# Performance work log

Hardware: AMD Instinct MI355X
Metric: run time of the kernel (lower is better)

The kernel has to match this reference:

```python
import jax, jax.numpy as jnp
import numpy as np

N_NODES = 100000
N_EDGES = 1600000
IN_FEATS = 128
HEADS = 4
OUT_FEATS = 32
NEG_SLOPE = 0.2


def setup_inputs() -> dict:
    key = jax.random.key(0)
    ks = jax.random.split(key, 7)
    x = jax.random.normal(ks[0], (N_NODES, IN_FEATS), dtype=jnp.float32)
    fc_w = jax.random.normal(ks[1], (HEADS * OUT_FEATS, IN_FEATS), dtype=jnp.float32) * (1.0 / np.sqrt(IN_FEATS))
    attn_l = jax.random.normal(ks[2], (HEADS, OUT_FEATS), dtype=jnp.float32) * (1.0 / np.sqrt(OUT_FEATS))
    attn_r = jax.random.normal(ks[3], (HEADS, OUT_FEATS), dtype=jnp.float32) * (1.0 / np.sqrt(OUT_FEATS))
    bias = jnp.zeros((HEADS * OUT_FEATS,), dtype=jnp.float32)
    src = jax.random.randint(ks[4], (N_EDGES,), 0, N_NODES, dtype=jnp.int64 if jax.config.jax_enable_x64 else jnp.int32)
    dst = jax.random.randint(ks[5], (N_EDGES,), 0, N_NODES, dtype=jnp.int64 if jax.config.jax_enable_x64 else jnp.int32)
    return {"x": x, "fc_w": fc_w, "attn_l": attn_l, "attn_r": attn_r, "bias": bias, "src": src, "dst": dst}


def reference(x, fc_w, attn_l, attn_r, bias, src, dst):
    """DGL GATConv (feat_drop=attn_drop=0, residual identity since in==H*D,
    allow_zero_in_degree=True, activation=None), then concat heads."""
    N = x.shape[0]
    H, D = attn_l.shape
    # linear projection: [N, H, D]
    feat = (x @ fc_w.T).reshape(N, H, D)
    # per-node attention halves: [N, H]
    el = jnp.einsum('nhd,hd->nh', feat, attn_l)
    er = jnp.einsum('nhd,hd->nh', feat, attn_r)
    # per-edge score with leaky relu: [E, H]
    e = el[src] + er[dst]
    e = jnp.where(e > 0, e, NEG_SLOPE * e)
    # edge softmax grouped by destination node
    emax = jax.ops.segment_max(e, dst, num_segments=N)          # [N, H]
    ee = jnp.exp(e - emax[dst])                                  # [E, H]
    denom = jax.ops.segment_sum(ee, dst, num_segments=N)        # [N, H]
    a = ee / jnp.maximum(denom[dst], jnp.float32(1e-38))         # [E, H]
    # weighted message + scatter aggregate: [N, H, D]
    msg = feat[src] * a[:, :, None]
    rst = jax.ops.segment_sum(msg, dst, num_segments=N)
    # residual (identity since in_feats == H*D) + bias
    rst = rst + x.reshape(N, H, D) + bias.reshape(1, H, D)
    # concat heads
    return rst.reshape(N, H * D)
```

## Files before the change

kernel.cpp:

```cpp
#include <hip/hip_runtime.h>
#include <math.h>

#define NEG_SLOPE 0.2f
#define PB 256
#define BKT_SHIFT 8

typedef __attribute__((ext_vector_type(8))) short bf16x8;
typedef __attribute__((ext_vector_type(4))) float f32x4;

__device__ __forceinline__ unsigned bf16_rne(float f) {
  unsigned u = __float_as_uint(f);
  return (u + 0x7fff + ((u >> 16) & 1)) >> 16;
}

__device__ __forceinline__ float lrelu_exp(float v) {
  v = v > 0.f ? v : NEG_SLOPE * v;
  return __expf(v);
}

__device__ __forceinline__ void local_blk_scan(const int* __restrict__ blk_sums,
                                               int* s_blk_off, int nb, int t) {
  if (t < 64) {
    const int v = (t < nb) ? blk_sums[t] : 0;
    int incl = v;
#pragma unroll
    for (int d = 1; d < 64; d <<= 1) {
      const int o = __shfl_up(incl, d);
      if (t >= d) incl += o;
    }
    s_blk_off[t] = incl - v;
  }
}

__global__ __launch_bounds__(256) void gemm_feat_attn(
    const float* __restrict__ x, const unsigned* __restrict__ fc_wb,
    const float* __restrict__ attn_l, const float* __restrict__ attn_r,
    unsigned* __restrict__ featb, float* __restrict__ el,
    float* __restrict__ er, int N)
{
  __shared__ __align__(16) unsigned w_lds[128 * 68];
  const int t = threadIdx.x;
  const int row_base = blockIdx.x * 64;

  {
    const uint4* fb4 = reinterpret_cast<const uint4*>(fc_wb);
#pragma unroll
    for (int k = 0; k < 8; ++k) {
      const int i4 = t + k * 256;
      const uint4 v = fb4[i4];
      const int row = i4 >> 4;
      unsigned* d = &w_lds[row * 68 + (i4 & 15) * 4];
      d[0] = v.x; d[1] = v.y; d[2] = v.z; d[3] = v.w;
    }
  }

  const int w = t >> 6;
  const int l = t & 63;
  const int cl = l & 15;
  const int g = l >> 4;

  const int arow = min(row_base + w * 16 + cl, N - 1);
  const float* __restrict__ xp = x + (size_t)arow * 128;
  bf16x8 a_frag[4];
#pragma unroll
  for (int ks = 0; ks < 4; ++ks) {
    const float4 v0 = *reinterpret_cast<const float4*>(xp + ks * 32 + g * 8);
    const float4 v1 =
        *reinterpret_cast<const float4*>(xp + ks * 32 + g * 8 + 4);
    uint4 uu;
    uu.x = bf16_rne(v0.x) | (bf16_rne(v0.y) << 16);
    uu.y = bf16_rne(v0.z) | (bf16_rne(v0.w) << 16);
    uu.z = bf16_rne(v1.x) | (bf16_rne(v1.y) << 16);
    uu.w = bf16_rne(v1.z) | (bf16_rne(v1.w) << 16);
    a_frag[ks] = *reinterpret_cast<bf16x8*>(&uu);
  }
  __syncthreads();

  f32x4 acc[8];
#pragma unroll
  for (int ct = 0; ct < 8; ++ct) acc[ct] = (f32x4){0.f, 0.f, 0.f, 0.f};

#pragma unroll
  for (int ct = 0; ct < 8; ++ct) {
#pragma unroll
    for (int ks = 0; ks < 4; ++ks) {
      const bf16x8 b_frag = *reinterpret_cast<const bf16x8*>(
          &w_lds[(ct * 16 + cl) * 68 + ks * 16 + g * 4]);
      acc[ct] = __builtin_amdgcn_mfma_f32_16x16x32_bf16(a_frag[ks], b_frag,
                                                        acc[ct], 0, 0, 0);
    }
  }

#pragma unroll
  for (int ct = 0; ct < 8; ++ct) {
#pragma unroll
    for (int r = 0; r < 4; ++r) {
      const float v = acc[ct][r];
      const float vn = __shfl_xor(v, 1);
      const int node = row_base + w * 16 + g * 4 + r;
      if ((cl & 1) == 0 && node < N) {
        featb[(size_t)node * 64 + ct * 8 + (cl >> 1)] =
            bf16_rne(v) | (bf16_rne(vn) << 16);
      }
    }
  }

  float al_lo[4], al_hi[4], ar_lo[4], ar_hi[4];
#pragma unroll
  for (int h = 0; h < 4; ++h) {
    al_lo[h] = attn_l[h * 32 + cl];
    al_hi[h] = attn_l[h * 32 + 16 + cl];
    ar_lo[h] = attn_r[h * 32 + cl];
    ar_hi[h] = attn_r[h * 32 + 16 + cl];
  }
#pragma unroll
  for (int r = 0; r < 4; ++r) {
    const int node = row_base + w * 16 + g * 4 + r;
#pragma unroll
    for (int h = 0; h < 4; ++h) {
      float pl = acc[2 * h][r] * al_lo[h] + acc[2 * h + 1][r] * al_hi[h];
      float pr = acc[2 * h][r] * ar_lo[h] + acc[2 * h + 1][r] * ar_hi[h];
#pragma unroll
      for (int d = 1; d < 16; d <<= 1) {
        pl += __shfl_xor(pl, d);
        pr += __shfl_xor(pr, d);
      }
      if (cl == 0 && node < N) {
        el[(size_t)node * 4 + h] = pl;
        er[(size_t)node * 4 + h] = pr;
      }
    }
  }
}

__global__ __launch_bounds__(256) void hist_bucket(const int* __restrict__ dst,
                                                   int* __restrict__ hist,
                                                   const float* __restrict__ fc_w,
                                                   unsigned* __restrict__ fc_wb,
                                                   int E, int NB, int chunk) {
  __shared__ int h[512];
  const int k = blockIdx.x, t = threadIdx.x;
  if (k < 32) {
    const int i = k * 256 + t;
    const float2 v = reinterpret_cast<const float2*>(fc_w)[i];
    fc_wb[i] = bf16_rne(v.x) | (bf16_rne(v.y) << 16);
  }
  for (int i = t; i < NB; i += 256) h[i] = 0;
  __syncthreads();
  const int beg = k * chunk, end = min(E, beg + chunk);
  for (int e = beg + t; e < end; e += 256)
    atomicAdd(&h[dst[e] >> BKT_SHIFT], 1);
  __syncthreads();
  for (int i = t; i < NB; i += 256) hist[i * PB + k] = h[i];
}

__global__ __launch_bounds__(256) void scan_a(const int* __restrict__ deg,
                                              int* __restrict__ offs,
                                              int* __restrict__ blk_sums,
                                              int n) {
  __shared__ int wsum[4];
  const int b = blockIdx.x, t = threadIdx.x;
  const int base = b * 2048 + t * 8;
  int v[8];
  int s = 0;
#pragma unroll
  for (int j = 0; j < 8; ++j) {
    v[j] = s;
    const int d = (base + j < n) ? deg[base + j] : 0;
    s += d;
  }
  const int lane = t & 63;
  int incl = s;
#pragma unroll
  for (int d = 1; d < 64; d <<= 1) {
    const int o = __shfl_up(incl, d);
    if (lane >= d) incl += o;
  }
  const int w = t >> 6;
  if (lane == 63) wsum[w] = incl;
  __syncthreads();
  int woff = 0;
  for (int ww = 0; ww < w; ++ww) woff += wsum[ww];
  const int thr_excl = woff + incl - s;
#pragma unroll
  for (int j = 0; j < 8; ++j)
    if (base + j < n) offs[base + j] = thr_excl + v[j];
  if (t == 255) blk_sums[b] = woff + incl;
}

__global__ __launch_bounds__(256) void part_scatter(
    const int* __restrict__ src, const int* __restrict__ dst,
    const int* __restrict__ hscan, const int* __restrict__ blk_sums,
    unsigned* __restrict__ part, int E, int NB, int chunk, int nb) {
  __shared__ int cur[512];
  __shared__ int s_blk_off[64];
  const int k = blockIdx.x, t = threadIdx.x;
  local_blk_scan(blk_sums, s_blk_off, nb, t);
  __syncthreads();
  for (int i = t; i < NB; i += 256) {
    const int m = i * PB + k;
    cur[i] = hscan[m] + s_blk_off[m >> 11];
  }
  __syncthreads();
  const int beg = k * chunk, end = min(E, beg + chunk);
  for (int e = beg + t; e < end; e += 256) {
    const int d = dst[e];
    const int b = d >> BKT_SHIFT;
    const int pos = atomicAdd(&cur[b], 1);
    part[pos] = (unsigned)src[e] |
                ((unsigned)(d & ((1 << BKT_SHIFT) - 1)) << 20);
  }
}

__global__ __launch_bounds__(512) void build_csr(
    const unsigned* __restrict__ part, const int* __restrict__ hscan,
    const int* __restrict__ blk_sums, const float* __restrict__ el,
    const float* __restrict__ er, int* __restrict__ node_offs,
    unsigned* __restrict__ csr, uint2* __restrict__ wsb,
    int N, int E, int NB, int nb) {
  __shared__ int cnt[256];
  __shared__ int wtot[4];
  __shared__ int s_blk_off[64];
  const int b = blockIdx.x, t = threadIdx.x;
  local_blk_scan(blk_sums, s_blk_off, nb, t);
  if (t < 256) cnt[t] = 0;
  __syncthreads();
  const int m0 = b * PB;
  const int bbase = hscan[m0] + s_blk_off[m0 >> 11];
  int bend = E;
  if (b + 1 < NB) {
    const int m1 = (b + 1) * PB;
    bend = hscan[m1] + s_blk_off[m1 >> 11];
  }
  const int node0 = b << BKT_SHIFT;
  for (int p = bbase + t; p < bend; p += 512)
    atomicAdd(&cnt[part[p] >> 20], 1);
  __syncthreads();
  int a0 = 0, incl = 0;
  if (t < 256) {
    a0 = cnt[t];
    incl = a0;
#pragma unroll
    for (int d1 = 1; d1 < 64; d1 <<= 1) {
      const int o = __shfl_up(incl, d1);
      if ((t & 63) >= d1) incl += o;
    }
    if ((t & 63) == 63) wtot[t >> 6] = incl;
  }
  __syncthreads();
  if (t < 256) {
    const int w = t >> 6;
    int woff = 0;
    for (int ww = 0; ww < w; ++ww) woff += wtot[ww];
    const int e0 = woff + incl - a0;
    cnt[t] = e0;
    if (node0 + t < N) node_offs[node0 + t] = bbase + e0;
    if (b == NB - 1 && t == 0) node_offs[N] = E;
  }
  __syncthreads();
  for (int p = bbase + t; p < bend; p += 512) {
    const unsigned v = part[p];
    const int lpos = atomicAdd(&cnt[v >> 20], 1);
    csr[bbase + lpos] = v;
  }
  __syncthreads();
  for (int p = bbase + t; p < bend; p += 512) {
    const unsigned v = csr[p];
    const unsigned s = v & 0xFFFFFu;
    const unsigned ld = v >> 20;
    const float4 l4 = *reinterpret_cast<const float4*>(el + s * 4);
    const float4 r4 =
        *reinterpret_cast<const float4*>(er + (unsigned)(node0 + ld) * 4);
    uint2 u;
    u.x = bf16_rne(lrelu_exp(l4.x + r4.x)) |
          (bf16_rne(lrelu_exp(l4.y + r4.y)) << 16);
    u.y = bf16_rne(lrelu_exp(l4.z + r4.z)) |
          (bf16_rne(lrelu_exp(l4.w + r4.w)) << 16);
    wsb[p] = u;
  }
}

__global__ __launch_bounds__(256) void agg_kernel(
    const uint4* __restrict__ featb4, const unsigned* __restrict__ csr,
    const unsigned short* __restrict__ wsb_us, const float* __restrict__ x,
    const float* __restrict__ bias, const int* __restrict__ node_offs,
    float* __restrict__ out, int N, int E)
{
  const int n = (int)((blockIdx.x * (size_t)blockDim.x + threadIdx.x) >> 6);
  if (n >= N) return;
  const unsigned lane = threadIdx.x & 63;
  const unsigned q = lane >> 4;
  const unsigned li = lane & 15;
  const unsigned hh = li >> 2;
  const unsigned short* __restrict__ wp = wsb_us + hh;
  const int beg = node_offs[n];
  const int end = node_offs[n + 1];
  const int nfull = (end - beg) >> 4;

  float a0 = 0.f, a1 = 0.f, a2 = 0.f, a3 = 0.f;
  float a4 = 0.f, a5 = 0.f, a6 = 0.f, a7 = 0.f, ds = 0.f;
  int p = beg;
  for (int gi = 0; gi < nfull; ++gi, p += 16) {
    unsigned pk[4]; unsigned wu[4]; uint4 fv[4];
#pragma unroll
    for (int i = 0; i < 4; ++i) pk[i] = csr[(unsigned)p + 4 * i + q];
#pragma unroll
    for (int i = 0; i < 4; ++i)
      wu[i] = wp[((unsigned)p + 4 * i + q) * 4];
#pragma unroll
    for (int i = 0; i < 4; ++i)
      fv[i] = featb4[(pk[i] & 0xFFFFFu) * 16 + li];
#pragma unroll
    for (int i = 0; i < 4; ++i) {
      const float w = __uint_as_float(wu[i] << 16);
      a0 = fmaf(w, __uint_as_float(fv[i].x << 16), a0);
      a1 = fmaf(w, __uint_as_float(fv[i].x & 0xffff0000u), a1);
      a2 = fmaf(w, __uint_as_float(fv[i].y << 16), a2);
      a3 = fmaf(w, __uint_as_float(fv[i].y & 0xffff0000u), a3);
      a4 = fmaf(w, __uint_as_float(fv[i].z << 16), a4);
      a5 = fmaf(w, __uint_as_float(fv[i].z & 0xffff0000u), a5);
      a6 = fmaf(w, __uint_as_float(fv[i].w << 16), a6);
      a7 = fmaf(w, __uint_as_float(fv[i].w & 0xffff0000u), a7);
      ds += w;
    }
  }
  if (p < end) {
    const int last = end - 1;
    unsigned pk[4]; unsigned wu[4]; uint4 fv[4]; int ee[4];
#pragma unroll
    for (int i = 0; i < 4; ++i) ee[i] = p + 4 * i + (int)q;
#pragma unroll
    for (int i = 0; i < 4; ++i) pk[i] = csr[(unsigned)min(ee[i], last)];
#pragma unroll
    for (int i = 0; i < 4; ++i)
      wu[i] = wp[(unsigned)min(ee[i], last) * 4];
#pragma unroll
    for (int i = 0; i < 4; ++i)
      fv[i] = featb4[(pk[i] & 0xFFFFFu) * 16 + li];
#pragma unroll
    for (int i = 0; i < 4; ++i) {
      float w = __uint_as_float(wu[i] << 16);
      if (ee[i] > last) w = 0.f;
      a0 = fmaf(w, __uint_as_float(fv[i].x << 16), a0);
      a1 = fmaf(w, __uint_as_float(fv[i].x & 0xffff0000u), a1);
      a2 = fmaf(w, __uint_as_float(fv[i].y << 16), a2);
      a3 = fmaf(w, __uint_as_float(fv[i].y & 0xffff0000u), a3);
      a4 = fmaf(w, __uint_as_float(fv[i].z << 16), a4);
      a5 = fmaf(w, __uint_as_float(fv[i].z & 0xffff0000u), a5);
      a6 = fmaf(w, __uint_as_float(fv[i].w << 16), a6);
      a7 = fmaf(w, __uint_as_float(fv[i].w & 0xffff0000u), a7);
      ds += w;
    }
  }

  a0 += __shfl_xor(a0, 16); a0 += __shfl_xor(a0, 32);
  a1 += __shfl_xor(a1, 16); a1 += __shfl_xor(a1, 32);
  a2 += __shfl_xor(a2, 16); a2 += __shfl_xor(a2, 32);
  a3 += __shfl_xor(a3, 16); a3 += __shfl_xor(a3, 32);
  a4 += __shfl_xor(a4, 16); a4 += __shfl_xor(a4, 32);
  a5 += __shfl_xor(a5, 16); a5 += __shfl_xor(a5, 32);
  a6 += __shfl_xor(a6, 16); a6 += __shfl_xor(a6, 32);
  a7 += __shfl_xor(a7, 16); a7 += __shfl_xor(a7, 32);
  ds += __shfl_xor(ds, 16); ds += __shfl_xor(ds, 32);

  if (q == 0) {
    const float inv = 1.f / fmaxf(ds, 1e-38f);
    const float4 x0 = ((const float4*)x)[(unsigned)n * 32 + 2 * li];
    const float4 x1 = ((const float4*)x)[(unsigned)n * 32 + 2 * li + 1];
    const float4 b0 = ((const float4*)bias)[2 * li];
    const float4 b1 = ((const float4*)bias)[2 * li + 1];
    float4 o0, o1;
    o0.x = fmaf(a0, inv, x0.x + b0.x);
    o0.y = fmaf(a1, inv, x0.y + b0.y);
    o0.z = fmaf(a2, inv, x0.z + b0.z);
    o0.w = fmaf(a3, inv, x0.w + b0.w);
    o1.x = fmaf(a4, inv, x1.x + b1.x);
    o1.y = fmaf(a5, inv, x1.y + b1.y);
    o1.z = fmaf(a6, inv, x1.z + b1.z);
    o1.w = fmaf(a7, inv, x1.w + b1.w);
    ((float4*)out)[(unsigned)n * 32 + 2 * li] = o0;
    ((float4*)out)[(unsigned)n * 32 + 2 * li + 1] = o1;
  }
}

extern "C" void kernel_launch(void* const* d_in, const int* in_sizes, int n_in,
                              void* d_out, int out_size, void* d_ws,
                              size_t ws_size, hipStream_t stream) {
  const float* x      = (const float*)d_in[0];
  const float* fc_w   = (const float*)d_in[1];
  const float* attn_l = (const float*)d_in[2];
  const float* attn_r = (const float*)d_in[3];
  const float* bias   = (const float*)d_in[4];
  const int*   src    = (const int*)d_in[5];
  const int*   dst    = (const int*)d_in[6];
  const int N = in_sizes[0] / 128;
  const int E = in_sizes[5];
  float* out = (float*)d_out;

  const int NB = (N + 255) >> 8;
  const int M = NB * PB;
  const int chunk = (E + PB - 1) / PB;
  const int nb = (M + 2047) / 2048;

  char* ws = (char*)d_ws;
  size_t off = 0;
  auto alloc = [&](size_t bytes) {
    void* p = ws + off;
    off += (bytes + 255) & ~(size_t)255;
    return p;
  };
  unsigned* featb   = (unsigned*)alloc((size_t)N * 128 * 2);
  unsigned* fc_wb   = (unsigned*)alloc(128 * 64 * 4);
  float* el         = (float*)alloc((size_t)N * 4 * 4);
  float* er         = (float*)alloc((size_t)N * 4 * 4);
  int*   hist       = (int*)alloc((size_t)M * 4);
  int*   hscan      = (int*)alloc((size_t)(M + 1) * 4);
  int*   node_offs  = (int*)alloc((size_t)(N + 1) * 4);
  int*   blk_sums   = (int*)alloc(256);
  unsigned* part    = (unsigned*)alloc((size_t)E * 4);
  unsigned* csr     = (unsigned*)alloc((size_t)E * 4);
  uint2* wsb        = (uint2*)alloc((size_t)E * 8);

  hist_bucket<<<PB, 256, 0, stream>>>(dst, hist, fc_w, fc_wb, E, NB, chunk);
  gemm_feat_attn<<<(N + 63) / 64, 256, 0, stream>>>(x, fc_wb, attn_l, attn_r,
                                                    featb, el, er, N);
  scan_a<<<nb, 256, 0, stream>>>(hist, hscan, blk_sums, M);
  part_scatter<<<PB, 256, 0, stream>>>(src, dst, hscan, blk_sums, part, E,
                                       NB, chunk, nb);
  build_csr<<<NB, 512, 0, stream>>>(part, hscan, blk_sums, el, er, node_offs,
                                    csr, wsb, N, E, NB, nb);
  agg_kernel<<<(N + 3) / 4, 256, 0, stream>>>((const uint4*)featb, csr,
                                              (const unsigned short*)wsb, x,
                                              bias, node_offs, out, N, E);
}
```

Measured before the change: 151.9 us.

## Fuse CSR-build stages into one cooperative kernel and merge histogram into GEMM

Merges the bucket histogram into the GEMM launch as extra trailing blocks, and has each GEMM block convert fc_w to bf16 itself instead of reading a preconverted buffer. The scan, partition scatter and CSR build become one cooperative kernel with grid-wide syncs, replacing four launches. The goal is to cut kernel launch and inter-kernel gap overhead. In exchange, part_scatter and build_csr now run on 256 blocks of 512 threads, looping over buckets instead of one block per bucket, which may lower parallelism, and grid.sync adds its own cost.

```diff
diff --git a/kernel.cpp b/kernel.cpp
--- a/kernel.cpp
+++ b/kernel.cpp
@@ -1,5 +1,8 @@
 #include <hip/hip_runtime.h>
+#include <hip/hip_cooperative_groups.h>
 #include <math.h>
+
+namespace cg = cooperative_groups;
 
 #define NEG_SLOPE 0.2f
 #define PB 256
@@ -18,39 +21,39 @@
   return __expf(v);
 }
 
-__device__ __forceinline__ void local_blk_scan(const int* __restrict__ blk_sums,
-                                               int* s_blk_off, int nb, int t) {
-  if (t < 64) {
-    const int v = (t < nb) ? blk_sums[t] : 0;
-    int incl = v;
-#pragma unroll
-    for (int d = 1; d < 64; d <<= 1) {
-      const int o = __shfl_up(incl, d);
-      if (t >= d) incl += o;
-    }
-    s_blk_off[t] = incl - v;
-  }
-}
-
-__global__ __launch_bounds__(256) void gemm_feat_attn(
-    const float* __restrict__ x, const unsigned* __restrict__ fc_wb,
+__global__ __launch_bounds__(256) void gemm_hist(
+    const float* __restrict__ x, const float* __restrict__ fc_w,
     const float* __restrict__ attn_l, const float* __restrict__ attn_r,
-    unsigned* __restrict__ featb, float* __restrict__ el,
-    float* __restrict__ er, int N)
+    const int* __restrict__ dst, unsigned* __restrict__ featb,
+    float* __restrict__ el, float* __restrict__ er, int* __restrict__ hist,
+    int N, int E, int NB, int chunk, int G)
 {
   __shared__ __align__(16) unsigned w_lds[128 * 68];
+  __shared__ int h[512];
   const int t = threadIdx.x;
+
+  if (blockIdx.x >= G) {
+    const int k = blockIdx.x - G;
+    for (int i = t; i < NB; i += 256) h[i] = 0;
+    __syncthreads();
+    const int beg = k * chunk, end = min(E, beg + chunk);
+    for (int e = beg + t; e < end; e += 256)
+      atomicAdd(&h[dst[e] >> BKT_SHIFT], 1);
+    __syncthreads();
+    for (int i = t; i < NB; i += 256) hist[i * PB + k] = h[i];
+    return;
+  }
+
   const int row_base = blockIdx.x * 64;
-
   {
-    const uint4* fb4 = reinterpret_cast<const uint4*>(fc_wb);
-#pragma unroll
-    for (int k = 0; k < 8; ++k) {
-      const int i4 = t + k * 256;
-      const uint4 v = fb4[i4];
-      const int row = i4 >> 4;
-      unsigned* d = &w_lds[row * 68 + (i4 & 15) * 4];
-      d[0] = v.x; d[1] = v.y; d[2] = v.z; d[3] = v.w;
+    const int c = t >> 1, half = t & 1;
+    const float* src = fc_w + (size_t)c * 128 + half * 64;
+    unsigned* dstp = &w_lds[c * 68 + half * 32];
+#pragma unroll
+    for (int i = 0; i < 16; ++i) {
+      const float4 v = *reinterpret_cast<const float4*>(src + i * 4);
+      dstp[2 * i]     = bf16_rne(v.x) | (bf16_rne(v.y) << 16);
+      dstp[2 * i + 1] = bf16_rne(v.z) | (bf16_rne(v.w) << 16);
     }
   }
 
@@ -107,176 +110,172 @@
 
   float al_lo[4], al_hi[4], ar_lo[4], ar_hi[4];
 #pragma unroll
-  for (int h = 0; h < 4; ++h) {
-    al_lo[h] = attn_l[h * 32 + cl];
-    al_hi[h] = attn_l[h * 32 + 16 + cl];
-    ar_lo[h] = attn_r[h * 32 + cl];
-    ar_hi[h] = attn_r[h * 32 + 16 + cl];
+  for (int hh = 0; hh < 4; ++hh) {
+    al_lo[hh] = attn_l[hh * 32 + cl];
+    al_hi[hh] = attn_l[hh * 32 + 16 + cl];
+    ar_lo[hh] = attn_r[hh * 32 + cl];
+    ar_hi[hh] = attn_r[hh * 32 + 16 + cl];
   }
 #pragma unroll
   for (int r = 0; r < 4; ++r) {
     const int node = row_base + w * 16 + g * 4 + r;
 #pragma unroll
-    for (int h = 0; h < 4; ++h) {
-      float pl = acc[2 * h][r] * al_lo[h] + acc[2 * h + 1][r] * al_hi[h];
-      float pr = acc[2 * h][r] * ar_lo[h] + acc[2 * h + 1][r] * ar_hi[h];
+    for (int hh = 0; hh < 4; ++hh) {
+      float pl = acc[2 * hh][r] * al_lo[hh] + acc[2 * hh + 1][r] * al_hi[hh];
+      float pr = acc[2 * hh][r] * ar_lo[hh] + acc[2 * hh + 1][r] * ar_hi[hh];
 #pragma unroll
       for (int d = 1; d < 16; d <<= 1) {
         pl += __shfl_xor(pl, d);
         pr += __shfl_xor(pr, d);
       }
       if (cl == 0 && node < N) {
-        el[(size_t)node * 4 + h] = pl;
-        er[(size_t)node * 4 + h] = pr;
-      }
-    }
-  }
-}
-
-__global__ __launch_bounds__(256) void hist_bucket(const int* __restrict__ dst,
-                                                   int* __restrict__ hist,
-                                                   const float* __restrict__ fc_w,
-                                                   unsigned* __restrict__ fc_wb,
-                                                   int E, int NB, int chunk) {
-  __shared__ int h[512];
-  const int k = blockIdx.x, t = threadIdx.x;
-  if (k < 32) {
-    const int i = k * 256 + t;
-    const float2 v = reinterpret_cast<const float2*>(fc_w)[i];
-    fc_wb[i] = bf16_rne(v.x) | (bf16_rne(v.y) << 16);
-  }
-  for (int i = t; i < NB; i += 256) h[i] = 0;
-  __syncthreads();
-  const int beg = k * chunk, end = min(E, beg + chunk);
-  for (int e = beg + t; e < end; e += 256)
-    atomicAdd(&h[dst[e] >> BKT_SHIFT], 1);
-  __syncthreads();
-  for (int i = t; i < NB; i += 256) hist[i * PB + k] = h[i];
-}
-
-__global__ __launch_bounds__(256) void scan_a(const int* __restrict__ deg,
-                                              int* __restrict__ offs,
-                                              int* __restrict__ blk_sums,
-                                              int n) {
-  __shared__ int wsum[4];
-  const int b = blockIdx.x, t = threadIdx.x;
-  const int base = b * 2048 + t * 8;
-  int v[8];
-  int s = 0;
-#pragma unroll
-  for (int j = 0; j < 8; ++j) {
-    v[j] = s;
-    const int d = (base + j < n) ? deg[base + j] : 0;
-    s += d;
-  }
-  const int lane = t & 63;
-  int incl = s;
-#pragma unroll
-  for (int d = 1; d < 64; d <<= 1) {
-    const int o = __shfl_up(incl, d);
-    if (lane >= d) incl += o;
-  }
-  const int w = t >> 6;
-  if (lane == 63) wsum[w] = incl;
-  __syncthreads();
-  int woff = 0;
-  for (int ww = 0; ww < w; ++ww) woff += wsum[ww];
-  const int thr_excl = woff + incl - s;
-#pragma unroll
-  for (int j = 0; j < 8; ++j)
-    if (base + j < n) offs[base + j] = thr_excl + v[j];
-  if (t == 255) blk_sums[b] = woff + incl;
-}
-
-__global__ __launch_bounds__(256) void part_scatter(
+        el[(size_t)node * 4 + hh] = pl;
+        er[(size_t)node * 4 + hh] = pr;
+      }
+    }
+  }
+}
+
+__global__ __launch_bounds__(512) void csr_coop(
     const int* __restrict__ src, const int* __restrict__ dst,
-    const int* __restrict__ hscan, const int* __restrict__ blk_sums,
-    unsigned* __restrict__ part, int E, int NB, int chunk, int nb) {
+    const int* __restrict__ hist, int* __restrict__ hscan,
+    int* __restrict__ blk_sums, const float* __restrict__ el,
+    const float* __restrict__ er, int* __restrict__ node_offs,
+    unsigned* __restrict__ part, unsigned* __restrict__ csr,
+    uint2* __restrict__ wsb, int N, int E, int NB, int chunk, int nb, int M)
+{
+  cg::grid_group grid = cg::this_grid();
   __shared__ int cur[512];
-  __shared__ int s_blk_off[64];
-  const int k = blockIdx.x, t = threadIdx.x;
-  local_blk_scan(blk_sums, s_blk_off, nb, t);
-  __syncthreads();
-  for (int i = t; i < NB; i += 256) {
-    const int m = i * PB + k;
-    cur[i] = hscan[m] + s_blk_off[m >> 11];
-  }
-  __syncthreads();
-  const int beg = k * chunk, end = min(E, beg + chunk);
-  for (int e = beg + t; e < end; e += 256) {
-    const int d = dst[e];
-    const int b = d >> BKT_SHIFT;
-    const int pos = atomicAdd(&cur[b], 1);
-    part[pos] = (unsigned)src[e] |
-                ((unsigned)(d & ((1 << BKT_SHIFT) - 1)) << 20);
-  }
-}
-
-__global__ __launch_bounds__(512) void build_csr(
-    const unsigned* __restrict__ part, const int* __restrict__ hscan,
-    const int* __restrict__ blk_sums, const float* __restrict__ el,
-    const float* __restrict__ er, int* __restrict__ node_offs,
-    unsigned* __restrict__ csr, uint2* __restrict__ wsb,
-    int N, int E, int NB, int nb) {
   __shared__ int cnt[256];
   __shared__ int wtot[4];
+  __shared__ int wsum[4];
   __shared__ int s_blk_off[64];
-  const int b = blockIdx.x, t = threadIdx.x;
-  local_blk_scan(blk_sums, s_blk_off, nb, t);
-  if (t < 256) cnt[t] = 0;
+  const int blk = blockIdx.x;
+  const int t = threadIdx.x;
+
+  {
+    const bool act = (blk < nb) && (t < 256);
+    int v[8]; int s = 0; int incl = 0;
+    if (act) {
+      const int base = blk * 2048 + t * 8;
+#pragma unroll
+      for (int j = 0; j < 8; ++j) {
+        v[j] = s;
+        const int d = (base + j < M) ? hist[base + j] : 0;
+        s += d;
+      }
+      incl = s;
+#pragma unroll
+      for (int d = 1; d < 64; d <<= 1) {
+        const int o = __shfl_up(incl, d);
+        if ((t & 63) >= d) incl += o;
+      }
+      if ((t & 63) == 63) wsum[t >> 6] = incl;
+    }
+    __syncthreads();
+    if (act) {
+      const int w = t >> 6;
+      int woff = 0;
+      for (int ww = 0; ww < w; ++ww) woff += wsum[ww];
+      const int thr_excl = woff + incl - s;
+      const int base = blk * 2048 + t * 8;
+#pragma unroll
+      for (int j = 0; j < 8; ++j)
+        if (base + j < M) hscan[base + j] = thr_excl + v[j];
+      if (t == 255) blk_sums[blk] = woff + incl;
+    }
+  }
+  __threadfence();
+  grid.sync();
+
+  if (t < 64) {
+    const int v = (t < nb) ? blk_sums[t] : 0;
+    int incl = v;
+#pragma unroll
+    for (int d = 1; d < 64; d <<= 1) {
+      const int o = __shfl_up(incl, d);
+      if (t >= d) incl += o;
+    }
+    s_blk_off[t] = incl - v;
+  }
   __syncthreads();
-  const int m0 = b * PB;
-  const int bbase = hscan[m0] + s_blk_off[m0 >> 11];
-  int bend = E;
-  if (b + 1 < NB) {
-    const int m1 = (b + 1) * PB;
-    bend = hscan[m1] + s_blk_off[m1 >> 11];
-  }
-  const int node0 = b << BKT_SHIFT;
-  for (int p = bbase + t; p < bend; p += 512)
-    atomicAdd(&cnt[part[p] >> 20], 1);
-  __syncthreads();
-  int a0 = 0, incl = 0;
-  if (t < 256) {
-    a0 = cnt[t];
-    incl = a0;
-#pragma unroll
-    for (int d1 = 1; d1 < 64; d1 <<= 1) {
-      const int o = __shfl_up(incl, d1);
-      if ((t & 63) >= d1) incl += o;
-    }
-    if ((t & 63) == 63) wtot[t >> 6] = incl;
-  }
-  __syncthreads();
-  if (t < 256) {
-    const int w = t >> 6;
-    int woff = 0;
-    for (int ww = 0; ww < w; ++ww) woff += wtot[ww];
-    const int e0 = woff + incl - a0;
-    cnt[t] = e0;
-    if (node0 + t < N) node_offs[node0 + t] = bbase + e0;
-    if (b == NB - 1 && t == 0) node_offs[N] = E;
-  }
-  __syncthreads();
-  for (int p = bbase + t; p < bend; p += 512) {
-    const unsigned v = part[p];
-    const int lpos = atomicAdd(&cnt[v >> 20], 1);
-    csr[bbase + lpos] = v;
-  }
-  __syncthreads();
-  for (int p = bbase + t; p < bend; p += 512) {
-    const unsigned v = csr[p];
-    const unsigned s = v & 0xFFFFFu;
-    const unsigned ld = v >> 20;
-    const float4 l4 = *reinterpret_cast<const float4*>(el + s * 4);
-    const float4 r4 =
-        *reinterpret_cast<const float4*>(er + (unsigned)(node0 + ld) * 4);
-    uint2 u;
-    u.x = bf16_rne(lrelu_exp(l4.x + r4.x)) |
-          (bf16_rne(lrelu_exp(l4.y + r4.y)) << 16);
-    u.y = bf16_rne(lrelu_exp(l4.z + r4.z)) |
-          (bf16_rne(lrelu_exp(l4.w + r4.w)) << 16);
-    wsb[p] = u;
+
+  {
+    const int k = blk;
+    for (int i = t; i < NB; i += 512) {
+      const int m = i * PB + k;
+      cur[i] = hscan[m] + s_blk_off[m >> 11];
+    }
+    __syncthreads();
+    const int beg = k * chunk, end = min(E, beg + chunk);
+    for (int e = beg + t; e < end; e += 512) {
+      const int d = dst[e];
+      const int b = d >> BKT_SHIFT;
+      const int pos = atomicAdd(&cur[b], 1);
+      part[pos] = (unsigned)src[e] |
+                  ((unsigned)(d & ((1 << BKT_SHIFT) - 1)) << 20);
+    }
+  }
+  __threadfence();
+  grid.sync();
+
+  for (int bb = blk; bb < NB; bb += PB) {
+    if (t < 256) cnt[t] = 0;
+    __syncthreads();
+    const int m0 = bb * PB;
+    const int bbase = hscan[m0] + s_blk_off[m0 >> 11];
+    int bend = E;
+    if (bb + 1 < NB) {
+      const int m1 = (bb + 1) * PB;
+      bend = hscan[m1] + s_blk_off[m1 >> 11];
+    }
+    const int node0 = bb << BKT_SHIFT;
+    for (int p = bbase + t; p < bend; p += 512)
+      atomicAdd(&cnt[part[p] >> 20], 1);
+    __syncthreads();
+    int a0 = 0, incl = 0;
+    if (t < 256) {
+      a0 = cnt[t];
+      incl = a0;
+#pragma unroll
+      for (int d1 = 1; d1 < 64; d1 <<= 1) {
+        const int o = __shfl_up(incl, d1);
+        if ((t & 63) >= d1) incl += o;
+      }
+      if ((t & 63) == 63) wtot[t >> 6] = incl;
+    }
+    __syncthreads();
+    if (t < 256) {
+      const int w = t >> 6;
+      int woff = 0;
+      for (int ww = 0; ww < w; ++ww) woff += wtot[ww];
+      const int e0 = woff + incl - a0;
+      cnt[t] = e0;
+      if (node0 + t < N) node_offs[node0 + t] = bbase + e0;
+      if (bb == NB - 1 && t == 0) node_offs[N] = E;
+    }
+    __syncthreads();
+    for (int p = bbase + t; p < bend; p += 512) {
+      const unsigned v = part[p];
+      const int lpos = atomicAdd(&cnt[v >> 20], 1);
+      csr[bbase + lpos] = v;
+    }
+    __syncthreads();
+    for (int p = bbase + t; p < bend; p += 512) {
+      const unsigned v = csr[p];
+      const unsigned s = v & 0xFFFFFu;
+      const unsigned ld = v >> 20;
+      const float4 l4 = *reinterpret_cast<const float4*>(el + s * 4);
+      const float4 r4 =
+          *reinterpret_cast<const float4*>(er + (unsigned)(node0 + ld) * 4);
+      uint2 u;
+      u.x = bf16_rne(lrelu_exp(l4.x + r4.x)) |
+            (bf16_rne(lrelu_exp(l4.y + r4.y)) << 16);
+      u.y = bf16_rne(lrelu_exp(l4.z + r4.z)) |
+            (bf16_rne(lrelu_exp(l4.w + r4.w)) << 16);
+      wsb[p] = u;
+    }
+    __syncthreads();
   }
 }
 
@@ -393,14 +392,14 @@
   const float* bias   = (const float*)d_in[4];
   const int*   src    = (const int*)d_in[5];
   const int*   dst    = (const int*)d_in[6];
-  const int N = in_sizes[0] / 128;
-  const int E = in_sizes[5];
+  int N = in_sizes[0] / 128;
+  int E = in_sizes[5];
   float* out = (float*)d_out;
 
-  const int NB = (N + 255) >> 8;
-  const int M = NB * PB;
-  const int chunk = (E + PB - 1) / PB;
-  const int nb = (M + 2047) / 2048;
+  int NB = (N + 255) >> 8;
+  int M = NB * PB;
+  int chunk = (E + PB - 1) / PB;
+  int nb = (M + 2047) / 2048;
 
   char* ws = (char*)d_ws;
   size_t off = 0;
@@ -410,7 +409,6 @@
     return p;
   };
   unsigned* featb   = (unsigned*)alloc((size_t)N * 128 * 2);
-  unsigned* fc_wb   = (unsigned*)alloc(128 * 64 * 4);
   float* el         = (float*)alloc((size_t)N * 4 * 4);
   float* er         = (float*)alloc((size_t)N * 4 * 4);
   int*   hist       = (int*)alloc((size_t)M * 4);
@@ -421,14 +419,18 @@
   unsigned* csr     = (unsigned*)alloc((size_t)E * 4);
   uint2* wsb        = (uint2*)alloc((size_t)E * 8);
 
-  hist_bucket<<<PB, 256, 0, stream>>>(dst, hist, fc_w, fc_wb, E, NB, chunk);
-  gemm_feat_attn<<<(N + 63) / 64, 256, 0, stream>>>(x, fc_wb, attn_l, attn_r,
-                                                    featb, el, er, N);
-  scan_a<<<nb, 256, 0, stream>>>(hist, hscan, blk_sums, M);
-  part_scatter<<<PB, 256, 0, stream>>>(src, dst, hscan, blk_sums, part, E,
-                                       NB, chunk, nb);
-  build_csr<<<NB, 512, 0, stream>>>(part, hscan, blk_sums, el, er, node_offs,
-                                    csr, wsb, N, E, NB, nb);
+  const int G = (N + 63) / 64;
+  gemm_hist<<<G + PB, 256, 0, stream>>>(x, fc_w, attn_l, attn_r, dst, featb,
+                                        el, er, hist, N, E, NB, chunk, G);
+
+  void* cargs[] = {(void*)&src, (void*)&dst, (void*)&hist, (void*)&hscan,
+                   (void*)&blk_sums, (void*)&el, (void*)&er,
+                   (void*)&node_offs, (void*)&part, (void*)&csr, (void*)&wsb,
+                   (void*)&N, (void*)&E, (void*)&NB, (void*)&chunk,
+                   (void*)&nb, (void*)&M};
+  hipLaunchCooperativeKernel((void*)csr_coop, dim3(PB), dim3(512), cargs, 0,
+                             stream);
+
   agg_kernel<<<(N + 3) / 4, 256, 0, stream>>>((const uint4*)featb, csr,
                                               (const unsigned short*)wsb, x,
                                               bias, node_offs, out, N, E);
```

After: 313.8 us. 2.07x slower.

## Fuse histogram kernel into GEMM launch and convert weights to bf16 per block

Applied to the files above, without the earlier changes.

Merges the destination-bucket histogram kernel into the feature-projection GEMM kernel by appending extra blocks that run the histogram, so the two independent stages share one launch and can overlap. Each GEMM block now converts the fp32 weight matrix to bf16 itself while loading it into LDS, which removes the separate fc_wb buffer and the dependency on the earlier kernel. The cost is redundant weight conversion in every GEMM block and extra LDS per block for the histogram array, which may reduce occupancy.

```diff
diff --git a/kernel.cpp b/kernel.cpp
--- a/kernel.cpp
+++ b/kernel.cpp
@@ -32,25 +32,39 @@
   }
 }
 
-__global__ __launch_bounds__(256) void gemm_feat_attn(
-    const float* __restrict__ x, const unsigned* __restrict__ fc_wb,
+__global__ __launch_bounds__(256) void gemm_hist(
+    const float* __restrict__ x, const float* __restrict__ fc_w,
     const float* __restrict__ attn_l, const float* __restrict__ attn_r,
-    unsigned* __restrict__ featb, float* __restrict__ el,
-    float* __restrict__ er, int N)
+    const int* __restrict__ dst, unsigned* __restrict__ featb,
+    float* __restrict__ el, float* __restrict__ er, int* __restrict__ hist,
+    int N, int E, int NB, int chunk, int G)
 {
   __shared__ __align__(16) unsigned w_lds[128 * 68];
+  __shared__ int h[512];
   const int t = threadIdx.x;
+
+  if (blockIdx.x >= G) {
+    const int k = blockIdx.x - G;
+    for (int i = t; i < NB; i += 256) h[i] = 0;
+    __syncthreads();
+    const int beg = k * chunk, end = min(E, beg + chunk);
+    for (int e = beg + t; e < end; e += 256)
+      atomicAdd(&h[dst[e] >> BKT_SHIFT], 1);
+    __syncthreads();
+    for (int i = t; i < NB; i += 256) hist[i * PB + k] = h[i];
+    return;
+  }
+
   const int row_base = blockIdx.x * 64;
-
   {
-    const uint4* fb4 = reinterpret_cast<const uint4*>(fc_wb);
-#pragma unroll
-    for (int k = 0; k < 8; ++k) {
-      const int i4 = t + k * 256;
-      const uint4 v = fb4[i4];
-      const int row = i4 >> 4;
-      unsigned* d = &w_lds[row * 68 + (i4 & 15) * 4];
-      d[0] = v.x; d[1] = v.y; d[2] = v.z; d[3] = v.w;
+    const int c = t >> 1, half = t & 1;
+    const float* src = fc_w + (size_t)c * 128 + half * 64;
+    unsigned* dstp = &w_lds[c * 68 + half * 32];
+#pragma unroll
+    for (int i = 0; i < 16; ++i) {
+      const float4 v = *reinterpret_cast<const float4*>(src + i * 4);
+      dstp[2 * i]     = bf16_rne(v.x) | (bf16_rne(v.y) << 16);
+      dstp[2 * i + 1] = bf16_rne(v.z) | (bf16_rne(v.w) << 16);
     }
   }
 
@@ -107,51 +121,30 @@
 
   float al_lo[4], al_hi[4], ar_lo[4], ar_hi[4];
 #pragma unroll
-  for (int h = 0; h < 4; ++h) {
-    al_lo[h] = attn_l[h * 32 + cl];
-    al_hi[h] = attn_l[h * 32 + 16 + cl];
-    ar_lo[h] = attn_r[h * 32 + cl];
-    ar_hi[h] = attn_r[h * 32 + 16 + cl];
+  for (int hh = 0; hh < 4; ++hh) {
+    al_lo[hh] = attn_l[hh * 32 + cl];
+    al_hi[hh] = attn_l[hh * 32 + 16 + cl];
+    ar_lo[hh] = attn_r[hh * 32 + cl];
+    ar_hi[hh] = attn_r[hh * 32 + 16 + cl];
   }
 #pragma unroll
   for (int r = 0; r < 4; ++r) {
     const int node = row_base + w * 16 + g * 4 + r;
 #pragma unroll
-    for (int h = 0; h < 4; ++h) {
-      float pl = acc[2 * h][r] * al_lo[h] + acc[2 * h + 1][r] * al_hi[h];
-      float pr = acc[2 * h][r] * ar_lo[h] + acc[2 * h + 1][r] * ar_hi[h];
+    for (int hh = 0; hh < 4; ++hh) {
+      float pl = acc[2 * hh][r] * al_lo[hh] + acc[2 * hh + 1][r] * al_hi[hh];
+      float pr = acc[2 * hh][r] * ar_lo[hh] + acc[2 * hh + 1][r] * ar_hi[hh];
 #pragma unroll
       for (int d = 1; d < 16; d <<= 1) {
         pl += __shfl_xor(pl, d);
         pr += __shfl_xor(pr, d);
       }
       if (cl == 0 && node < N) {
-        el[(size_t)node * 4 + h] = pl;
-        er[(size_t)node * 4 + h] = pr;
+        el[(size_t)node * 4 + hh] = pl;
+        er[(size_t)node * 4 + hh] = pr;
       }
     }
   }
-}
-
-__global__ __launch_bounds__(256) void hist_bucket(const int* __restrict__ dst,
-                                                   int* __restrict__ hist,
-                                                   const float* __restrict__ fc_w,
-                                                   unsigned* __restrict__ fc_wb,
-                                                   int E, int NB, int chunk) {
-  __shared__ int h[512];
-  const int k = blockIdx.x, t = threadIdx.x;
-  if (k < 32) {
-    const int i = k * 256 + t;
-    const float2 v = reinterpret_cast<const float2*>(fc_w)[i];
-    fc_wb[i] = bf16_rne(v.x) | (bf16_rne(v.y) << 16);
-  }
-  for (int i = t; i < NB; i += 256) h[i] = 0;
-  __syncthreads();
-  const int beg = k * chunk, end = min(E, beg + chunk);
-  for (int e = beg + t; e < end; e += 256)
-    atomicAdd(&h[dst[e] >> BKT_SHIFT], 1);
-  __syncthreads();
-  for (int i = t; i < NB; i += 256) hist[i * PB + k] = h[i];
 }
 
 __global__ __launch_bounds__(256) void scan_a(const int* __restrict__ deg,
@@ -410,7 +403,6 @@
     return p;
   };
   unsigned* featb   = (unsigned*)alloc((size_t)N * 128 * 2);
-  unsigned* fc_wb   = (unsigned*)alloc(128 * 64 * 4);
   float* el         = (float*)alloc((size_t)N * 4 * 4);
   float* er         = (float*)alloc((size_t)N * 4 * 4);
   int*   hist       = (int*)alloc((size_t)M * 4);
@@ -421,9 +413,9 @@
   unsigned* csr     = (unsigned*)alloc((size_t)E * 4);
   uint2* wsb        = (uint2*)alloc((size_t)E * 8);
 
-  hist_bucket<<<PB, 256, 0, stream>>>(dst, hist, fc_w, fc_wb, E, NB, chunk);
-  gemm_feat_attn<<<(N + 63) / 64, 256, 0, stream>>>(x, fc_wb, attn_l, attn_r,
-                                                    featb, el, er, N);
+  const int G = (N + 63) / 64;
+  gemm_hist<<<G + PB, 256, 0, stream>>>(x, fc_w, attn_l, attn_r, dst, featb,
+                                        el, er, hist, N, E, NB, chunk, G);
   scan_a<<<nb, 256, 0, stream>>>(hist, hscan, blk_sums, M);
   part_scatter<<<PB, 256, 0, stream>>>(src, dst, hscan, blk_sums, part, E,
                                        NB, chunk, nb);
```

New measurement: 152.8 us. No clear change (+0.6%).
